# Optimization experiments

Hardware: AMD Instinct MI355X
Metric: run time of the kernel (lower is better)

Reference implementation:

```python
import jax, jax.numpy as jnp
import numpy as np

N = 4096          # n_neurons
M = 10            # max_memory
T = 10            # max_ticks
B = 1024          # batch
P = N // 2 // 2   # n_pairs = 1024
AD = 64           # attention_dim


def ln(x, g, b, eps=1e-5):
    m = x.mean(-1, keepdims=True)
    v = ((x - m) ** 2).mean(-1, keepdims=True)
    return (x - m) * jax.lax.rsqrt(v + eps) * g + b


def setup_inputs() -> dict:
    key = jax.random.key(0)
    ks = iter(jax.random.split(key, 64))

    def rn(shape, s=0.05):
        return (jax.random.normal(next(ks), shape) * s).astype(jnp.float32)

    d = {}
    d['x'] = jax.random.normal(next(ks), (B, 1, 28, 28), dtype=jnp.float32)
    d['post0'] = jax.random.normal(next(ks), (N, M), dtype=jnp.float32)
    d['pre0'] = jax.random.normal(next(ks), (N, M), dtype=jnp.float32)
    d['pairs'] = jax.random.randint(next(ks), (P, 2), 0, N)
    d['decay'] = jnp.full((P,), 0.1, jnp.float32)
    # image encoder: 784 -> 128 -> 32 -> 4
    d['ie_w1'] = rn((784, 128)); d['ie_b1'] = jnp.zeros(128); d['ie_g1'] = jnp.ones(128); d['ie_be1'] = jnp.zeros(128)
    d['ie_w2'] = rn((128, 32));  d['ie_b2'] = jnp.zeros(32);  d['ie_g2'] = jnp.ones(32);  d['ie_be2'] = jnp.zeros(32)
    d['ie_w3'] = rn((32, 4));    d['ie_b3'] = jnp.zeros(4)
    # synapse model: (4+N) -> 256 -> N
    d['sy_w1'] = rn((4 + N, 256)); d['sy_b1'] = jnp.zeros(256); d['sy_g'] = jnp.ones(256); d['sy_be'] = jnp.zeros(256)
    d['sy_w2'] = rn((256, N));     d['sy_b2'] = jnp.zeros(N)
    # batched per-neuron models: M -> 128 -> 1
    d['nm_w1'] = rn((N, M, 128)); d['nm_b1'] = jnp.zeros((N, 128))
    d['nm_g'] = jnp.ones((N, 128)); d['nm_be'] = jnp.zeros((N, 128))
    d['nm_w2'] = rn((N, 128));    d['nm_b2'] = jnp.zeros(N)
    # attention projections
    d['key_w'] = rn((4, AD)); d['key_b'] = jnp.zeros(AD)
    d['val_w'] = rn((4, AD)); d['val_b'] = jnp.zeros(AD)
    d['q_w'] = rn((P, AD));   d['q_b'] = jnp.zeros(AD)
    # syncronization reader: (AD+P) -> 512 -> 64 -> 10
    d['rd_w1'] = rn((AD + P, 512)); d['rd_b1'] = jnp.zeros(512); d['rd_g1'] = jnp.ones(512); d['rd_be1'] = jnp.zeros(512)
    d['rd_w2'] = rn((512, 64));     d['rd_b2'] = jnp.zeros(64);  d['rd_g2'] = jnp.ones(64);  d['rd_be2'] = jnp.zeros(64)
    d['rd_w3'] = rn((64, 10));      d['rd_b3'] = jnp.zeros(10)
    return d


def reference(x, post0, pre0, pairs, decay,
              ie_w1, ie_b1, ie_g1, ie_be1, ie_w2, ie_b2, ie_g2, ie_be2, ie_w3, ie_b3,
              sy_w1, sy_b1, sy_g, sy_be, sy_w2, sy_b2,
              nm_w1, nm_b1, nm_g, nm_be, nm_w2, nm_b2,
              key_w, key_b, val_w, val_b, q_w, q_b,
              rd_w1, rd_b1, rd_g1, rd_be1, rd_w2, rd_b2, rd_g2, rd_be2, rd_w3, rd_b3):
    b = x.shape[0]
    fx = x.reshape(b, -1)
    # image encoder
    e = jax.nn.relu(ln(fx @ ie_w1 + ie_b1, ie_g1, ie_be1))
    e = jax.nn.relu(ln(e @ ie_w2 + ie_b2, ie_g2, ie_be2))
    enc = e @ ie_w3 + ie_b3                               # [B,4]
    keys = enc @ key_w + key_b                            # [B,AD]
    values = enc @ val_w + val_b                          # [B,AD]
    post, pre = post0, pre0
    pred = None
    for tick in range(T):
        last_post = jnp.broadcast_to(post[:, -1][None, :], (b, N))
        syn_in = jnp.concatenate([enc, last_post], axis=1)            # [B,4+N]
        h = jax.nn.relu(ln(syn_in @ sy_w1 + sy_b1, sy_g, sy_be))
        new_pre = h @ sy_w2 + sy_b2                                   # [B,N]
        pre = jnp.concatenate([pre[:, 1:], new_pre.mean(0)[:, None]], axis=1)
        # batched per-neuron MLP over history
        h2 = jax.nn.relu(ln(jnp.einsum('nm,nmh->nh', pre, nm_w1) + nm_b1, nm_g, nm_be))
        new_post = jnp.einsum('nh,nh->n', h2, nm_w2) + nm_b2          # [N]
        post = jnp.concatenate([post[:, 1:], new_post[:, None]], axis=1)
        # decayed pair synchronization
        L = min(tick + 1, M)
        Zi = post[pairs[:, 0], M - L:]                                # [P,L]
        Zj = post[pairs[:, 1], M - L:]
        td = jnp.arange(L - 1, -1, -1, dtype=post.dtype)              # [L]
        R = jnp.exp(-decay[:, None] * td[None, :])                    # [P,L]
        sync = jnp.sum(Zi * R * Zj, axis=1) / (jnp.sum(R, axis=1) + 1e-8)  # [P]
        sv = jnp.broadcast_to(sync[None, :], (b, P))                  # [B,P]
        q = sv @ q_w + q_b                                            # [B,AD]
        scores = jnp.sum(q * keys, axis=-1, keepdims=True) / jnp.sqrt(jnp.float32(AD))
        aw = jax.nn.softmax(scores, axis=-1)                          # [B,1] -> ones
        att = aw * values                                             # [B,AD]
        comb = jnp.concatenate([att, sv], axis=-1)                    # [B,AD+P]
        r = jax.nn.relu(ln(comb @ rd_w1 + rd_b1, rd_g1, rd_be1))
        r = jax.nn.relu(ln(r @ rd_w2 + rd_b2, rd_g2, rd_be2))
        pred = r @ rd_w3 + rd_b3                                      # [B,10]
    return pred
```

## Files before the change

kernel.cpp:

```cpp
#include <hip/hip_runtime.h>

#define N_ 4096
#define M_ 10
#define T_ 10
#define B_ 1024
#define P_ 1024
#define NBLK 256
#define NTHR 512

__device__ __forceinline__ float wave_red_sum(float v) {
#pragma unroll
  for (int m = 32; m >= 1; m >>= 1) v += __shfl_xor(v, m);
  return v;
}

__device__ __forceinline__ float gld(const float* p) {
  return __hip_atomic_load(p, __ATOMIC_RELAXED, __HIP_MEMORY_SCOPE_AGENT);
}
__device__ __forceinline__ void gst(float* p, float v) {
  __hip_atomic_store(p, v, __ATOMIC_RELAXED, __HIP_MEMORY_SCOPE_AGENT);
}
__device__ __forceinline__ unsigned ld_u(unsigned* p) {
  return __hip_atomic_load(p, __ATOMIC_RELAXED, __HIP_MEMORY_SCOPE_AGENT);
}

__device__ __forceinline__ void drain_sync() {
  asm volatile("s_waitcnt vmcnt(0)" ::: "memory");
  __syncthreads();
}
__device__ __forceinline__ void signal(unsigned* slot, unsigned val) {
  if (threadIdx.x == 0)
    __hip_atomic_store(slot, val, __ATOMIC_RELAXED, __HIP_MEMORY_SCOPE_AGENT);
}
__device__ __forceinline__ void wait_set(unsigned* slots, int n, unsigned target) {
  if (threadIdx.x < 64) {
    int lane = threadIdx.x;
    bool ok;
    do {
      ok = true;
      for (int i = lane; i < n; i += 64) ok &= (ld_u(&slots[i]) >= target);
      ok = __all(ok);
      if (!ok) __builtin_amdgcn_s_sleep(1);
    } while (!ok);
  }
  __syncthreads();
}
__device__ __forceinline__ void wait_mod8(unsigned* slots, int s, unsigned target) {
  if (threadIdx.x < 64) {
    int lane = threadIdx.x;
    bool ok;
    do {
      ok = (lane < 32) ? (ld_u(&slots[s + 8 * lane]) >= target) : true;
      ok = __all(ok);
      if (!ok) __builtin_amdgcn_s_sleep(1);
    } while (!ok);
  }
  __syncthreads();
}

__global__ void k_init(unsigned* __restrict__ bar) {
  if (threadIdx.x < 1024)
    __hip_atomic_store(bar + threadIdx.x, 0u, __ATOMIC_RELAXED, __HIP_MEMORY_SCOPE_AGENT);
}

struct MArgs {
  const float *x, *post0, *pre0;
  const int* pairs;
  const float* decay;
  const float *iew1, *ieb1, *ieg1, *iebe1, *iew2, *ieb2, *ieg2, *iebe2, *iew3, *ieb3;
  const float *syw1, *syb1, *syg, *sybe, *syw2, *syb2;
  const float *nw1, *nb1, *ng, *nbe, *nw2, *nb2;
  const float *vw, *vb;
  const float *rdw1, *rdb1, *rdg1, *rdbe1, *rdw2, *rdb2, *rdg2, *rdbe2, *rdw3, *rdb3;
  float *pc, *pc2, *enc_g, *hbar, *postG, *scp;
  float* out;
  unsigned* bar;
};

__global__ __launch_bounds__(NTHR)
void k_mega(MArgs a) {
  const int g = blockIdx.x, tid = threadIdx.x;
  const int lane = tid & 63;
  const int n0 = g * 16, b0e = g * 4;

  __shared__ float s_w1[16 * M_ * 128];
  __shared__ float s_syw1[16 * 256];
  __shared__ float s_w4[4 * 256];
  __shared__ float reg1[4096];
  __shared__ float reg2[1024];
  __shared__ float s_mbrb[2048];
  __shared__ float s_values[4][64];
  __shared__ float s_post[16][M_];
  __shared__ float s_pre[16][M_];
  __shared__ float s_pl[16];
  __shared__ float s_hbar[256];
  __shared__ float s_cval[256];
  __shared__ float s_tmp[2][256];
  __shared__ float s_stats[20];

  unsigned* slotA = a.bar;
  unsigned* slotR = a.bar + 256;
  unsigned* slotC = a.bar + 320;

  {
    const float4* src = (const float4*)(a.nw1 + n0 * M_ * 128);
    float4* dst = (float4*)s_w1;
    for (int i = tid; i < 16 * M_ * 128 / 4; i += NTHR) dst[i] = src[i];
    const float4* s2 = (const float4*)(a.syw1 + (4 + n0) * 256);
    float4* d2 = (float4*)s_syw1;
    for (int i = tid; i < 16 * 256 / 4; i += NTHR) d2[i] = s2[i];
    const float4* s3 = (const float4*)a.syw1;
    float4* d3 = (float4*)s_w4;
    for (int i = tid; i < 1024 / 4; i += NTHR) d3[i] = s3[i];
    if (tid < 160) {
      int r = tid / 10, m = tid - r * 10;
      s_post[r][m] = a.post0[(n0 + r) * M_ + m];
      s_pre[r][m]  = a.pre0[(n0 + r) * M_ + m];
    }
    for (int i = tid; i < 4 * 784; i += NTHR) reg1[i] = a.x[b0e * 784 + i];
  }
  __syncthreads();
  if (tid < 16) s_pl[tid] = s_post[tid][M_ - 1];

  {
    int r = tid >> 7, j = tid & 127;
    float u = a.ieb1[j];
    const float* fxr = reg1 + r * 784;
    for (int k = 0; k < 784; ++k) u += fxr[k] * a.iew1[k * 128 + j];
    float s = wave_red_sum(u), sq = wave_red_sum(u * u);
    int w = tid >> 6;
    if (lane == 0) { s_tmp[0][w] = s; s_tmp[1][w] = sq; }
    __syncthreads();
    float S = s_tmp[0][r * 2] + s_tmp[0][r * 2 + 1];
    float S2 = s_tmp[1][r * 2] + s_tmp[1][r * 2 + 1];
    float mm = S * (1.f / 128.f), vv = S2 * (1.f / 128.f) - mm * mm;
    reg2[r * 128 + j] = fmaxf((u - mm) * rsqrtf(vv + 1e-5f) * a.ieg1[j] + a.iebe1[j], 0.f);
  }
  __syncthreads();
  if (tid < 128) {
    int r = tid >> 5, jj = tid & 31;
    float u = a.ieb2[jj];
    for (int k = 0; k < 128; ++k) u += reg2[r * 128 + k] * a.iew2[k * 32 + jj];
    float ss = u, sq = u * u;
#pragma unroll
    for (int m = 16; m >= 1; m >>= 1) { ss += __shfl_xor(ss, m, 32); sq += __shfl_xor(sq, m, 32); }
    float mm = ss * (1.f / 32.f), vv = sq * (1.f / 32.f) - mm * mm;
    reg2[512 + r * 32 + jj] = fmaxf((u - mm) * rsqrtf(vv + 1e-5f) * a.ieg2[jj] + a.iebe2[jj], 0.f);
  }
  __syncthreads();
  if (tid < 16) {
    int r = tid >> 2, o = tid & 3;
    float u = a.ieb3[o];
    for (int k = 0; k < 32; ++k) u += reg2[512 + r * 32 + k] * a.iew3[k * 4 + o];
    reg2[640 + r * 4 + o] = u;
    gst(&a.enc_g[(b0e + r) * 4 + o], u);
  }
  __syncthreads();
  if (tid < 256) {
    int r = tid >> 6, v = tid & 63;
    float u = a.vb[v];
#pragma unroll
    for (int o = 0; o < 4; ++o) u += reg2[640 + r * 4 + o] * a.vw[o * 64 + v];
    s_values[r][v] = u;
  }
  __syncthreads();
  {
    int j = tid & 255, half = tid >> 8;
    float acc = 0.f;
#pragma unroll
    for (int r = 0; r < 8; ++r) {
      int n = half * 8 + r;
      acc += s_pl[n] * s_syw1[n * 256 + j];
    }
    s_tmp[half][j] = acc;
  }
  __syncthreads();
  if (tid < 256) gst(&a.pc[g * 256 + tid], s_tmp[0][tid] + s_tmp[1][tid]);
  drain_sync();
  signal(&slotA[g], 1u);

  {
    float q[14];
    if (tid < 256) {
      float wv[4] = {s_w4[tid], s_w4[256 + tid], s_w4[512 + tid], s_w4[768 + tid]};
      int idx = 0;
#pragma unroll
      for (int o = 0; o < 4; ++o) q[idx++] = wv[o];
#pragma unroll
      for (int o = 0; o < 4; ++o)
#pragma unroll
        for (int p = 0; p <= o; ++p) q[idx++] = wv[o] * wv[p];
    } else {
#pragma unroll
      for (int i = 0; i < 14; ++i) q[i] = 0.f;
    }
#pragma unroll
    for (int i = 0; i < 14; ++i) q[i] = wave_red_sum(q[i]);
    int w = tid >> 6;
    if (lane == 0) {
#pragma unroll
      for (int i = 0; i < 14; ++i) s_tmp[1][w * 16 + i] = q[i];
    }
    __syncthreads();
    if (tid < 14) {
      float S = 0.f;
#pragma unroll
      for (int w2 = 0; w2 < 8; ++w2) S += s_tmp[1][w2 * 16 + tid];
      s_stats[6 + tid] = S * (1.f / 256.f);
    }
  }
  __syncthreads();

  for (int t = 0; t < T_; ++t) {
    if (g < 8) {
      wait_mod8(slotA, g, (unsigned)(t + 1));
      int j = tid & 255, half = tid >> 8;
      float acc = 0.f;
#pragma unroll
      for (int i = 0; i < 16; ++i) {
        int r = g + 8 * (half * 16 + i);
        acc += gld(&a.pc[r * 256 + j]);
      }
      s_tmp[half][j] = acc;
      __syncthreads();
      if (tid < 256) gst(&a.pc2[g * 256 + tid], s_tmp[0][tid] + s_tmp[1][tid]);
      drain_sync();
      signal(&slotR[g], (unsigned)(t + 1));
    }
    wait_set(slotR, 8, (unsigned)(t + 1));
    if (t == 0) {
      for (int i = tid; i < 4096; i += NTHR) {
        int b = i >> 2, o = i & 3;
        reg1[o * 1024 + b] = gld(&a.enc_g[i]);
      }
    }
    {
      float cv = 0.f;
      if (tid < 256) {
        cv = a.syb1[tid];
#pragma unroll
        for (int s = 0; s < 8; ++s) cv += gld(&a.pc2[s * 256 + tid]);
        s_cval[tid] = cv;
      }
      float p[6];
      if (tid < 256) {
        p[0] = cv; p[1] = cv * cv;
        p[2] = cv * s_w4[tid]; p[3] = cv * s_w4[256 + tid];
        p[4] = cv * s_w4[512 + tid]; p[5] = cv * s_w4[768 + tid];
      } else {
#pragma unroll
        for (int i = 0; i < 6; ++i) p[i] = 0.f;
      }
#pragma unroll
      for (int i = 0; i < 6; ++i) p[i] = wave_red_sum(p[i]);
      int w = tid >> 6;
      if (lane == 0) {
#pragma unroll
        for (int i = 0; i < 6; ++i) s_tmp[0][w * 8 + i] = p[i];
      }
      __syncthreads();
      if (tid < 6) {
        float S = 0.f;
#pragma unroll
        for (int w2 = 0; w2 < 8; ++w2) S += s_tmp[0][w2 * 8 + tid];
        s_stats[tid] = S * (1.f / 256.f);
      }
      __syncthreads();
    }
    {
#pragma unroll
      for (int h2 = 0; h2 < 2; ++h2) {
        int b = h2 * 512 + tid;
        float e0 = reg1[b], e1v = reg1[1024 + b], e2v = reg1[2048 + b], e3v = reg1[3072 + b];
        float m = s_stats[0] + e0 * s_stats[6] + e1v * s_stats[7] + e2v * s_stats[8] + e3v * s_stats[9];
        float eu2 = s_stats[1] + 2.f * (e0 * s_stats[2] + e1v * s_stats[3] + e2v * s_stats[4] + e3v * s_stats[5]);
        float qf = e0 * e0 * s_stats[10]
                 + 2.f * e1v * e0 * s_stats[11] + e1v * e1v * s_stats[12]
                 + 2.f * e2v * e0 * s_stats[13] + 2.f * e2v * e1v * s_stats[14] + e2v * e2v * s_stats[15]
                 + 2.f * e3v * e0 * s_stats[16] + 2.f * e3v * e1v * s_stats[17]
                 + 2.f * e3v * e2v * s_stats[18] + e3v * e3v * s_stats[19];
        eu2 += qf;
        s_mbrb[b] = m;
        s_mbrb[1024 + b] = rsqrtf(eu2 - m * m + 1e-5f);
      }
      __syncthreads();
    }
    {
      float cj = s_cval[g];
      float w0 = s_w4[g], w1v = s_w4[256 + g], w2v = s_w4[512 + g], w3v = s_w4[768 + g];
      float gj = a.syg[g], bj = a.sybe[g];
      float acc = 0.f;
#pragma unroll
      for (int h2 = 0; h2 < 2; ++h2) {
        int b = h2 * 512 + tid;
        float u = cj + reg1[b] * w0 + reg1[1024 + b] * w1v + reg1[2048 + b] * w2v + reg1[3072 + b] * w3v;
        float y = (u - s_mbrb[b]) * s_mbrb[1024 + b] * gj + bj;
        acc += fmaxf(y, 0.f);
      }
      acc = wave_red_sum(acc);
      int w = tid >> 6;
      if (lane == 0) s_tmp[0][w] = acc;
      __syncthreads();
      if (tid == 0) {
        float S = 0.f;
#pragma unroll
        for (int w2 = 0; w2 < 8; ++w2) S += s_tmp[0][w2];
        gst(&a.hbar[g], S * (1.f / 1024.f));
      }
    }
    drain_sync();
    signal(&slotC[g], (unsigned)(t + 1));
    wait_set(slotC, 256, (unsigned)(t + 1));
    if (tid < 256) s_hbar[tid] = gld(&a.hbar[tid]);
    __syncthreads();
    {
      int nl = tid & 15, kq = tid >> 4;
      float u = 0.f;
#pragma unroll
      for (int kk = 0; kk < 8; ++kk) {
        int k = kq * 8 + kk;
        u += s_hbar[k] * a.syw2[k * N_ + n0 + nl];
      }
      ((float*)s_tmp)[kq * 16 + nl] = u;
    }
    __syncthreads();
    if (tid < 16) {
      float v = a.syb2[n0 + tid];
#pragma unroll
      for (int q2 = 0; q2 < 32; ++q2) v += ((float*)s_tmp)[q2 * 16 + tid];
#pragma unroll
      for (int m = 0; m < M_ - 1; ++m) s_pre[tid][m] = s_pre[tid][m + 1];
      s_pre[tid][M_ - 1] = v;
    }
    __syncthreads();
    {
      int nl = tid >> 5, q = tid & 31;
      int n2 = n0 + nl;
      float pr[M_];
#pragma unroll
      for (int m = 0; m < M_; ++m) pr[m] = s_pre[nl][m];
      float u[4];
#pragma unroll
      for (int k = 0; k < 4; ++k) {
        int j = q + 32 * k;
        float uu = a.nb1[n2 * 128 + j];
#pragma unroll
        for (int m = 0; m < M_; ++m) uu += pr[m] * s_w1[(nl * M_ + m) * 128 + j];
        u[k] = uu;
      }
      float s = u[0] + u[1] + u[2] + u[3];
      float sq = u[0] * u[0] + u[1] * u[1] + u[2] * u[2] + u[3] * u[3];
#pragma unroll
      for (int m = 16; m >= 1; m >>= 1) { s += __shfl_xor(s, m, 32); sq += __shfl_xor(sq, m, 32); }
      float mm = s * (1.f / 128.f), vv = sq * (1.f / 128.f) - mm * mm;
      float ri = rsqrtf(vv + 1e-5f);
      float d = 0.f;
#pragma unroll
      for (int k = 0; k < 4; ++k) {
        int j = q + 32 * k;
        float y = fmaxf((u[k] - mm) * ri * a.ng[n2 * 128 + j] + a.nbe[n2 * 128 + j], 0.f);
        d += y * a.nw2[n2 * 128 + j];
      }
#pragma unroll
      for (int m = 16; m >= 1; m >>= 1) d += __shfl_xor(d, m, 32);
      if (q == 0) {
        float npost = d + a.nb2[n2];
#pragma unroll
        for (int m = 0; m < M_ - 1; ++m) s_post[nl][m] = s_post[nl][m + 1];
        s_post[nl][M_ - 1] = npost;
        s_pl[nl] = npost;
      }
    }
    __syncthreads();
    if (t < T_ - 1) {
      int j = tid & 255, half = tid >> 8;
      float acc = 0.f;
#pragma unroll
      for (int r = 0; r < 8; ++r) {
        int n = half * 8 + r;
        acc += s_pl[n] * s_syw1[n * 256 + j];
      }
      s_tmp[half][j] = acc;
      __syncthreads();
      if (tid < 256) gst(&a.pc[g * 256 + tid], s_tmp[0][tid] + s_tmp[1][tid]);
    } else {
      if (tid < 160) {
        int r = tid / 10, m = tid - r * 10;
        gst(&a.postG[(n0 + r) * M_ + m], s_post[r][m]);
      }
    }
    drain_sync();
    signal(&slotA[g], (unsigned)(t + 2));
  }

  if (g < 8) {
    wait_set(slotA, 256, 11u);
    if (tid < 128) {
      int p = g * 128 + tid;
      int i = a.pairs[p * 2], jn = a.pairs[p * 2 + 1];
      float dc = a.decay[p];
      float num = 0.f, den = 0.f;
#pragma unroll
      for (int l = 0; l < M_; ++l) {
        float r = expf(-dc * (float)(M_ - 1 - l));
        num += gld(&a.postG[i * M_ + l]) * r * gld(&a.postG[jn * M_ + l]);
        den += r;
      }
      s_tmp[0][tid] = num / (den + 1e-8f);
    }
    __syncthreads();
    float acc = 0.f;
    for (int i = 0; i < 128; ++i)
      acc += s_tmp[0][i] * a.rdw1[(64 + g * 128 + i) * 512 + tid];
    gst(&a.scp[g * 512 + tid], acc);
    drain_sync();
    signal(&slotR[g], 11u);
  }
  wait_set(slotR, 8, 11u);
  {
    float* r1 = reg1;
    float* p2 = reg1 + 2048;
    float base = a.rdb1[tid];
#pragma unroll
    for (int s = 0; s < 8; ++s) base += gld(&a.scp[s * 512 + tid]);
    float u[4];
#pragma unroll
    for (int r = 0; r < 4; ++r) u[r] = base;
    for (int k = 0; k < 64; ++k) {
      float w = a.rdw1[k * 512 + tid];
#pragma unroll
      for (int r = 0; r < 4; ++r) u[r] += s_values[r][k] * w;
    }
    int wid = tid >> 6;
#pragma unroll
    for (int r = 0; r < 4; ++r) {
      float s = wave_red_sum(u[r]), sq = wave_red_sum(u[r] * u[r]);
      if (lane == 0) { s_tmp[0][r * 8 + wid] = s; s_tmp[1][r * 8 + wid] = sq; }
    }
    __syncthreads();
    float gg = a.rdg1[tid], bb = a.rdbe1[tid];
#pragma unroll
    for (int r = 0; r < 4; ++r) {
      float S = 0.f, S2 = 0.f;
#pragma unroll
      for (int w = 0; w < 8; ++w) { S += s_tmp[0][r * 8 + w]; S2 += s_tmp[1][r * 8 + w]; }
      float m = S * (1.f / 512.f), v = S2 * (1.f / 512.f) - m * m;
      r1[r * 512 + tid] = fmaxf((u[r] - m) * rsqrtf(v + 1e-5f) * gg + bb, 0.f);
    }
    __syncthreads();
    int o = tid & 63, kq = tid >> 6;
    float u2[4] = {0.f, 0.f, 0.f, 0.f};
#pragma unroll
    for (int kk = 0; kk < 64; ++kk) {
      int k = kq * 64 + kk;
      float w = a.rdw2[k * 64 + o];
#pragma unroll
      for (int r = 0; r < 4; ++r) u2[r] += r1[r * 512 + k] * w;
    }
#pragma unroll
    for (int r = 0; r < 4; ++r) p2[(kq * 4 + r) * 64 + o] = u2[r];
    __syncthreads();
    if (tid < 256) {
      int r = tid >> 6, o2 = tid & 63;
      float v = a.rdb2[o2];
#pragma unroll
      for (int q = 0; q < 8; ++q) v += p2[(q * 4 + r) * 64 + o2];
      float s = wave_red_sum(v), sq = wave_red_sum(v * v);
      float m = s * (1.f / 64.f), var = sq * (1.f / 64.f) - m * m;
      reg2[r * 64 + o2] = fmaxf((v - m) * rsqrtf(var + 1e-5f) * a.rdg2[o2] + a.rdbe2[o2], 0.f);
    }
    __syncthreads();
    if (tid < 40) {
      int r = tid / 10, o3 = tid - r * 10;
      float acc = a.rdb3[o3];
#pragma unroll
      for (int k = 0; k < 64; ++k) acc += reg2[r * 64 + k] * a.rdw3[k * 10 + o3];
      a.out[(b0e + r) * 10 + o3] = acc;
    }
  }
}

extern "C" void kernel_launch(void* const* d_in, const int* in_sizes, int n_in,
                              void* d_out, int out_size, void* d_ws, size_t ws_size,
                              hipStream_t stream) {
  MArgs a;
  a.x     = (const float*)d_in[0];
  a.post0 = (const float*)d_in[1];
  a.pre0  = (const float*)d_in[2];
  a.pairs = (const int*)d_in[3];
  a.decay = (const float*)d_in[4];
  a.iew1  = (const float*)d_in[5];
  a.ieb1  = (const float*)d_in[6];
  a.ieg1  = (const float*)d_in[7];
  a.iebe1 = (const float*)d_in[8];
  a.iew2  = (const float*)d_in[9];
  a.ieb2  = (const float*)d_in[10];
  a.ieg2  = (const float*)d_in[11];
  a.iebe2 = (const float*)d_in[12];
  a.iew3  = (const float*)d_in[13];
  a.ieb3  = (const float*)d_in[14];
  a.syw1  = (const float*)d_in[15];
  a.syb1  = (const float*)d_in[16];
  a.syg   = (const float*)d_in[17];
  a.sybe  = (const float*)d_in[18];
  a.syw2  = (const float*)d_in[19];
  a.syb2  = (const float*)d_in[20];
  a.nw1   = (const float*)d_in[21];
  a.nb1   = (const float*)d_in[22];
  a.ng    = (const float*)d_in[23];
  a.nbe   = (const float*)d_in[24];
  a.nw2   = (const float*)d_in[25];
  a.nb2   = (const float*)d_in[26];
  a.vw    = (const float*)d_in[29];
  a.vb    = (const float*)d_in[30];
  a.rdw1  = (const float*)d_in[33];
  a.rdb1  = (const float*)d_in[34];
  a.rdg1  = (const float*)d_in[35];
  a.rdbe1 = (const float*)d_in[36];
  a.rdw2  = (const float*)d_in[37];
  a.rdb2  = (const float*)d_in[38];
  a.rdg2  = (const float*)d_in[39];
  a.rdbe2 = (const float*)d_in[40];
  a.rdw3  = (const float*)d_in[41];
  a.rdb3  = (const float*)d_in[42];
  a.out = (float*)d_out;

  float* ws = (float*)d_ws;
  a.pc    = ws;
  a.pc2   = ws + 65536;
  a.enc_g = ws + 67584;
  a.hbar  = ws + 71680;
  a.postG = ws + 71936;
  a.scp   = ws + 112896;
  a.bar   = (unsigned*)(ws + 117000);

  k_init<<<1, 1024, 0, stream>>>(a.bar);
  k_mega<<<NBLK, NTHR, 0, stream>>>(a);
}
```

Before: 194.2 us.

## Cache syw2 slice in LDS, vectorize per-neuron MLP and encoding loads, simplify waits

Each block's 256x16 slice of syw2 is preloaded into shared memory once, replacing strided global reads on every tick. The per-neuron MLP now uses float4 loads of weights, gains and biases, and the encoder array is stored interleaved so one float4 read fetches all four values. The pc2 partial-sum read is split across both thread halves. The reducer blocks now wait on all 256 slotA slots instead of a mod-8 subset, which adds polling and synchronisation latency in the critical path.

Measured after the change: 203.8 us. 1.05x slower.

```diff
diff --git a/kernel.cpp b/kernel.cpp
--- a/kernel.cpp
+++ b/kernel.cpp
@@ -39,18 +39,6 @@
     do {
       ok = true;
       for (int i = lane; i < n; i += 64) ok &= (ld_u(&slots[i]) >= target);
-      ok = __all(ok);
-      if (!ok) __builtin_amdgcn_s_sleep(1);
-    } while (!ok);
-  }
-  __syncthreads();
-}
-__device__ __forceinline__ void wait_mod8(unsigned* slots, int s, unsigned target) {
-  if (threadIdx.x < 64) {
-    int lane = threadIdx.x;
-    bool ok;
-    do {
-      ok = (lane < 32) ? (ld_u(&slots[s + 8 * lane]) >= target) : true;
       ok = __all(ok);
       if (!ok) __builtin_amdgcn_s_sleep(1);
     } while (!ok);
@@ -86,6 +74,7 @@
   __shared__ float s_w1[16 * M_ * 128];
   __shared__ float s_syw1[16 * 256];
   __shared__ float s_w4[4 * 256];
+  __shared__ float s_syw2[256 * 16];
   __shared__ float reg1[4096];
   __shared__ float reg2[1024];
   __shared__ float s_mbrb[2048];
@@ -112,6 +101,11 @@
     const float4* s3 = (const float4*)a.syw1;
     float4* d3 = (float4*)s_w4;
     for (int i = tid; i < 1024 / 4; i += NTHR) d3[i] = s3[i];
+    for (int i = tid; i < 256 * 4; i += NTHR) {
+      int k = i >> 2, part = i & 3;
+      *(float4*)&s_syw2[k * 16 + part * 4] =
+          *(const float4*)&a.syw2[k * N_ + n0 + part * 4];
+    }
     if (tid < 160) {
       int r = tid / 10, m = tid - r * 10;
       s_post[r][m] = a.post0[(n0 + r) * M_ + m];
@@ -213,7 +207,7 @@
 
   for (int t = 0; t < T_; ++t) {
     if (g < 8) {
-      wait_mod8(slotA, g, (unsigned)(t + 1));
+      wait_set(slotA, 256, (unsigned)(t + 1));
       int j = tid & 255, half = tid >> 8;
       float acc = 0.f;
 #pragma unroll
@@ -229,17 +223,20 @@
     }
     wait_set(slotR, 8, (unsigned)(t + 1));
     if (t == 0) {
-      for (int i = tid; i < 4096; i += NTHR) {
-        int b = i >> 2, o = i & 3;
-        reg1[o * 1024 + b] = gld(&a.enc_g[i]);
-      }
-    }
+      for (int i = tid; i < 4096; i += NTHR) reg1[i] = gld(&a.enc_g[i]);
+    }
+    {
+      int j = tid & 255, half = tid >> 8;
+      float cp = 0.f;
+#pragma unroll
+      for (int s = 0; s < 4; ++s) cp += gld(&a.pc2[(half * 4 + s) * 256 + j]);
+      s_tmp[half][j] = cp;
+    }
+    __syncthreads();
     {
       float cv = 0.f;
       if (tid < 256) {
-        cv = a.syb1[tid];
-#pragma unroll
-        for (int s = 0; s < 8; ++s) cv += gld(&a.pc2[s * 256 + tid]);
+        cv = a.syb1[tid] + s_tmp[0][tid] + s_tmp[1][tid];
         s_cval[tid] = cv;
       }
       float p[6];
@@ -251,6 +248,7 @@
 #pragma unroll
         for (int i = 0; i < 6; ++i) p[i] = 0.f;
       }
+      __syncthreads();
 #pragma unroll
       for (int i = 0; i < 6; ++i) p[i] = wave_red_sum(p[i]);
       int w = tid >> 6;
@@ -271,17 +269,17 @@
 #pragma unroll
       for (int h2 = 0; h2 < 2; ++h2) {
         int b = h2 * 512 + tid;
-        float e0 = reg1[b], e1v = reg1[1024 + b], e2v = reg1[2048 + b], e3v = reg1[3072 + b];
-        float m = s_stats[0] + e0 * s_stats[6] + e1v * s_stats[7] + e2v * s_stats[8] + e3v * s_stats[9];
-        float eu2 = s_stats[1] + 2.f * (e0 * s_stats[2] + e1v * s_stats[3] + e2v * s_stats[4] + e3v * s_stats[5]);
-        float qf = e0 * e0 * s_stats[10]
-                 + 2.f * e1v * e0 * s_stats[11] + e1v * e1v * s_stats[12]
-                 + 2.f * e2v * e0 * s_stats[13] + 2.f * e2v * e1v * s_stats[14] + e2v * e2v * s_stats[15]
-                 + 2.f * e3v * e0 * s_stats[16] + 2.f * e3v * e1v * s_stats[17]
-                 + 2.f * e3v * e2v * s_stats[18] + e3v * e3v * s_stats[19];
+        float4 e = *(const float4*)&reg1[b * 4];
+        float m = s_stats[0] + e.x * s_stats[6] + e.y * s_stats[7] + e.z * s_stats[8] + e.w * s_stats[9];
+        float eu2 = s_stats[1] + 2.f * (e.x * s_stats[2] + e.y * s_stats[3] + e.z * s_stats[4] + e.w * s_stats[5]);
+        float qf = e.x * e.x * s_stats[10]
+                 + 2.f * e.y * e.x * s_stats[11] + e.y * e.y * s_stats[12]
+                 + 2.f * e.z * e.x * s_stats[13] + 2.f * e.z * e.y * s_stats[14] + e.z * e.z * s_stats[15]
+                 + 2.f * e.w * e.x * s_stats[16] + 2.f * e.w * e.y * s_stats[17]
+                 + 2.f * e.w * e.z * s_stats[18] + e.w * e.w * s_stats[19];
         eu2 += qf;
-        s_mbrb[b] = m;
-        s_mbrb[1024 + b] = rsqrtf(eu2 - m * m + 1e-5f);
+        s_mbrb[b * 2] = m;
+        s_mbrb[b * 2 + 1] = rsqrtf(eu2 - m * m + 1e-5f);
       }
       __syncthreads();
     }
@@ -293,8 +291,9 @@
 #pragma unroll
       for (int h2 = 0; h2 < 2; ++h2) {
         int b = h2 * 512 + tid;
-        float u = cj + reg1[b] * w0 + reg1[1024 + b] * w1v + reg1[2048 + b] * w2v + reg1[3072 + b] * w3v;
-        float y = (u - s_mbrb[b]) * s_mbrb[1024 + b] * gj + bj;
+        float4 e = *(const float4*)&reg1[b * 4];
+        float u = cj + e.x * w0 + e.y * w1v + e.z * w2v + e.w * w3v;
+        float y = (u - s_mbrb[b * 2]) * s_mbrb[b * 2 + 1] * gj + bj;
         acc += fmaxf(y, 0.f);
       }
       acc = wave_red_sum(acc);
@@ -319,7 +318,7 @@
 #pragma unroll
       for (int kk = 0; kk < 8; ++kk) {
         int k = kq * 8 + kk;
-        u += s_hbar[k] * a.syw2[k * N_ + n0 + nl];
+        u += s_hbar[k] * s_syw2[k * 16 + nl];
       }
       ((float*)s_tmp)[kq * 16 + nl] = u;
     }
@@ -336,31 +335,31 @@
     {
       int nl = tid >> 5, q = tid & 31;
       int n2 = n0 + nl;
+      int jb = q * 4;
       float pr[M_];
 #pragma unroll
       for (int m = 0; m < M_; ++m) pr[m] = s_pre[nl][m];
-      float u[4];
-#pragma unroll
-      for (int k = 0; k < 4; ++k) {
-        int j = q + 32 * k;
-        float uu = a.nb1[n2 * 128 + j];
-#pragma unroll
-        for (int m = 0; m < M_; ++m) uu += pr[m] * s_w1[(nl * M_ + m) * 128 + j];
-        u[k] = uu;
-      }
-      float s = u[0] + u[1] + u[2] + u[3];
-      float sq = u[0] * u[0] + u[1] * u[1] + u[2] * u[2] + u[3] * u[3];
+      float4 uu = *(const float4*)&a.nb1[n2 * 128 + jb];
+#pragma unroll
+      for (int m = 0; m < M_; ++m) {
+        float4 w = *(const float4*)&s_w1[(nl * M_ + m) * 128 + jb];
+        uu.x += pr[m] * w.x; uu.y += pr[m] * w.y;
+        uu.z += pr[m] * w.z; uu.w += pr[m] * w.w;
+      }
+      float s = uu.x + uu.y + uu.z + uu.w;
+      float sq = uu.x * uu.x + uu.y * uu.y + uu.z * uu.z + uu.w * uu.w;
 #pragma unroll
       for (int m = 16; m >= 1; m >>= 1) { s += __shfl_xor(s, m, 32); sq += __shfl_xor(sq, m, 32); }
       float mm = s * (1.f / 128.f), vv = sq * (1.f / 128.f) - mm * mm;
       float ri = rsqrtf(vv + 1e-5f);
-      float d = 0.f;
-#pragma unroll
-      for (int k = 0; k < 4; ++k) {
-        int j = q + 32 * k;
-        float y = fmaxf((u[k] - mm) * ri * a.ng[n2 * 128 + j] + a.nbe[n2 * 128 + j], 0.f);
-        d += y * a.nw2[n2 * 128 + j];
-      }
+      float4 gg = *(const float4*)&a.ng[n2 * 128 + jb];
+      float4 be = *(const float4*)&a.nbe[n2 * 128 + jb];
+      float4 w2v = *(const float4*)&a.nw2[n2 * 128 + jb];
+      float y0 = fmaxf((uu.x - mm) * ri * gg.x + be.x, 0.f);
+      float y1 = fmaxf((uu.y - mm) * ri * gg.y + be.y, 0.f);
+      float y2 = fmaxf((uu.z - mm) * ri * gg.z + be.z, 0.f);
+      float y3 = fmaxf((uu.w - mm) * ri * gg.w + be.w, 0.f);
+      float d = y0 * w2v.x + y1 * w2v.y + y2 * w2v.z + y3 * w2v.w;
 #pragma unroll
       for (int m = 16; m >= 1; m >>= 1) d += __shfl_xor(d, m, 32);
       if (q == 0) {
```
